# Optimization experiments

Hardware: AMD Instinct MI355X
Metric: run time of the kernel (lower is better)

## Reference

```python
import jax, jax.numpy as jnp
import numpy as np

N, VQ, VK, C, H = 4, 4096, 4096, 128, 64


def setup_inputs() -> dict:
    key = jax.random.key(0)
    kx, ky, kq, kk, kv = jax.random.split(key, 5)
    # xavier-uniform-ish scale for params
    def xavier(k, shape):
        fan_in, fan_out = shape
        lim = (6.0 / (fan_in + fan_out)) ** 0.5
        return jax.random.uniform(k, shape, jnp.float32, -lim, lim)
    return {
        "x": jax.random.normal(kx, (N, VQ, C), jnp.float32),
        "y": jax.random.normal(ky, (N, VK, C), jnp.float32),
        "Wq": xavier(kq, (C, H)),
        "Wk": xavier(kk, (C, H)),
        "Wv": xavier(kv, (C, C)),
    }


def reference(x, y, Wq, Wk, Wv):
    # x: [n, vq, c], y: [n, vk, c]
    scale = Wq.shape[1] ** (-0.5)
    q = jnp.einsum('nvc,co->nvo', x, Wq)   # [n, vq, h]
    k = jnp.einsum('nvc,co->nvo', y, Wk)   # [n, vk, h]
    v = jnp.einsum('nvc,co->nvo', y, Wv)   # [n, vk, c]
    scores = jnp.einsum('nqc,nkc->nqk', q, k) * scale  # [n, vq, vk]
    attn = jax.nn.softmax(scores, axis=-1)
    return jnp.einsum('nqk,nkc->nqc', attn, v)         # [n, vq, c]
```

## Files before the change

kernel.cpp:

```cpp
#include <hip/hip_runtime.h>

typedef __bf16 bf16x8 __attribute__((ext_vector_type(8)));
typedef __bf16 bf16x4 __attribute__((ext_vector_type(4)));
typedef __bf16 bf16x2 __attribute__((ext_vector_type(2)));
typedef float  f32x4  __attribute__((ext_vector_type(4)));
typedef float  f32x16 __attribute__((ext_vector_type(16)));
typedef int    i32x4  __attribute__((ext_vector_type(4)));

#define MFMA16 __builtin_amdgcn_mfma_f32_16x16x32_bf16
#define MFMA32 __builtin_amdgcn_mfma_f32_32x32x16_bf16

static constexpr int BATCH = 4;
static constexpr int SEQ   = 4096;
static constexpr int CDIM  = 128;
static constexpr int HDIM  = 64;
static constexpr float FIXMAX = 16.0f;

union FB2  { bf16x2 h; int i; };
union I4B8 { i32x4 i; bf16x8 b; };

__device__ inline bf16x8 load8f_cvt(const float* __restrict__ p) {
    f32x4 a = *reinterpret_cast<const f32x4*>(p);
    f32x4 b = *reinterpret_cast<const f32x4*>(p + 4);
    bf16x8 r;
    r[0] = (__bf16)a[0]; r[1] = (__bf16)a[1]; r[2] = (__bf16)a[2]; r[3] = (__bf16)a[3];
    r[4] = (__bf16)b[0]; r[5] = (__bf16)b[1]; r[6] = (__bf16)b[2]; r[7] = (__bf16)b[3];
    return r;
}


__global__ __launch_bounds__(256) void proj_all_kernel(
    const float* __restrict__ x, const float* __restrict__ y,
    const float* __restrict__ Wq, const float* __restrict__ Wk,
    const float* __restrict__ Wv,
    __bf16* __restrict__ Qw, __bf16* __restrict__ Kw, __bf16* __restrict__ Vtw,
    float qscale)
{
    __shared__ __bf16 Wt[64][136];
    __shared__ __bf16 Vtile[64][72];

    const int job = blockIdx.x >> 8;
    const int bx  = blockIdx.x & 255;
    const int t    = threadIdx.x;
    const int lane = t & 63;
    const int w    = t >> 6;
    const int m    = lane & 15;
    const int quad = lane >> 4;

    if (job <= 1) {
        const float* X    = job ? y  : x;
        const float* W    = job ? Wk : Wq;
        __bf16*      outp = job ? Kw : Qw;
        const float scale = job ? 1.0f : qscale;

        #pragma unroll
        for (int pass = 0; pass < 4; ++pass) {
            int flat = pass * 2048 + t * 8;
            int cin  = flat >> 6;
            int h0   = flat & 63;
            bf16x8 v = load8f_cvt(W + flat);
            #pragma unroll
            for (int j = 0; j < 8; ++j) Wt[h0 + j][cin] = v[j];
        }
        __syncthreads();

        const int row0 = bx * 64 + w * 16;
        bf16x8 af[4];
        #pragma unroll
        for (int kc = 0; kc < 4; ++kc)
            af[kc] = load8f_cvt(X + (long)(row0 + m) * 128 + kc * 32 + quad * 8);

        #pragma unroll
        for (int tn = 0; tn < 4; ++tn) {
            f32x4 acc = {0.f, 0.f, 0.f, 0.f};
            #pragma unroll
            for (int kc = 0; kc < 4; ++kc) {
                bf16x8 bfrag = *reinterpret_cast<const bf16x8*>(&Wt[tn * 16 + m][kc * 32 + quad * 8]);
                acc = MFMA16(af[kc], bfrag, acc, 0, 0, 0);
            }
            #pragma unroll
            for (int r = 0; r < 4; ++r) {
                int  kg   = row0 + quad * 4 + r;
                long addr = ((long)(kg >> 5) * 4 + tn) * 512
                          + ((m >> 3) * 32 + (kg & 31)) * 8 + (m & 7);
                outp[addr] = (__bf16)(acc[r] * scale);
            }
        }
    } else {
        const int cob = (job - 2) * 64;
        const int ct0 = (job - 2) * 2;

        #pragma unroll
        for (int pass = 0; pass < 4; ++pass) {
            int flat = pass * 2048 + t * 8;
            int cin  = flat >> 6;
            int co0  = flat & 63;
            bf16x8 v = load8f_cvt(Wv + cin * 128 + cob + co0);
            #pragma unroll
            for (int j = 0; j < 8; ++j) Wt[co0 + j][cin] = v[j];
        }
        __syncthreads();

        const int row0 = bx * 64 + w * 16;
        bf16x8 af[4];
        #pragma unroll
        for (int kc = 0; kc < 4; ++kc)
            af[kc] = load8f_cvt(y + (long)(row0 + m) * 128 + kc * 32 + quad * 8);

        #pragma unroll
        for (int tn = 0; tn < 4; ++tn) {
            f32x4 acc = {0.f, 0.f, 0.f, 0.f};
            #pragma unroll
            for (int kc = 0; kc < 4; ++kc) {
                bf16x8 bfrag = *reinterpret_cast<const bf16x8*>(&Wt[tn * 16 + m][kc * 32 + quad * 8]);
                acc = MFMA16(af[kc], bfrag, acc, 0, 0, 0);
            }
            bf16x4 pk;
            #pragma unroll
            for (int r = 0; r < 4; ++r) pk[r] = (__bf16)acc[r];
            *reinterpret_cast<bf16x4*>(&Vtile[tn * 16 + m][w * 16 + quad * 4]) = pk;
        }
        __syncthreads();

        #pragma unroll
        for (int pp = 0; pp < 2; ++pp) {
            int i       = pp * 256 + t;
            int c_local = i & 31;
            int hh      = (i >> 5) & 1;
            int kc2     = (i >> 6) & 1;
            int ct_l    = (i >> 7) & 1;
            int kt_l    = i >> 8;
            bf16x8 v = *reinterpret_cast<const bf16x8*>(
                &Vtile[ct_l * 32 + c_local][kt_l * 32 + kc2 * 16 + hh * 8]);
            long dst = ((long)(bx * 2 + kt_l) * 8 + (ct0 + ct_l) * 2 + kc2) * 512
                     + (hh * 32 + c_local) * 8;
            *reinterpret_cast<bf16x8*>(Vtw + dst) = v;
        }
    }
}

__global__ __launch_bounds__(512, 2) void attn_kernel(
    const __bf16* __restrict__ Qs, const __bf16* __restrict__ Ks,
    const __bf16* __restrict__ Vs, float* __restrict__ out)
{
    __shared__ __align__(16) char smem[98304];

    const int t    = threadIdx.x;
    const int lane = t & 63;
    const int w    = t >> 6;
    const int qh   = w & 1;
    const int g    = w >> 1;
    const int qc   = lane & 31;
    const int h    = lane >> 5;

    const int bx = blockIdx.x;
    const int n  = (bx >> 1) & 3;
    const int qt = (bx >> 3) * 2 + (bx & 1);
    const int q0 = qt * 64 + qh * 32;

    const long QT = (long)n * 128 + (q0 >> 5);
    bf16x8 qf[4];
    #pragma unroll
    for (int kc = 0; kc < 4; ++kc)
        qf[kc] = *reinterpret_cast<const bf16x8*>(Qs + (QT * 4 + kc) * 512 + lane * 8);

    const long KTg = (long)n * 128 + g * 32;
    const __bf16* sbase[6];
    int soff[6], sstep[6];
    if (qh == 0) {
        #pragma unroll
        for (int k = 0; k < 4; ++k) {
            sbase[k] = Ks + KTg * 2048 + k * 512 + lane * 8;
            soff[k]  = g * 4096 + k * 1024 + lane * 16;
            sstep[k] = 2048;
        }
        #pragma unroll
        for (int v2 = 0; v2 < 2; ++v2) {
            sbase[4 + v2] = Vs + KTg * 4096 + v2 * 512 + lane * 8;
            soff[4 + v2]  = 16384 + g * 8192 + v2 * 1024 + lane * 16;
            sstep[4 + v2] = 4096;
        }
    } else {
        #pragma unroll
        for (int v2 = 0; v2 < 6; ++v2) {
            sbase[v2] = Vs + KTg * 4096 + (v2 + 2) * 512 + lane * 8;
            soff[v2]  = 16384 + g * 8192 + (v2 + 2) * 1024 + lane * 16;
            sstep[v2] = 4096;
        }
    }

    f32x16 o_acc[4];
    #pragma unroll
    for (int ct = 0; ct < 4; ++ct)
        #pragma unroll
        for (int i = 0; i < 16; ++i) o_acc[ct][i] = 0.f;
    float l_a = 0.f, l_b = 0.f;

    bf16x8 stg[6];
    #pragma unroll
    for (int c = 0; c < 6; ++c) stg[c] = *reinterpret_cast<const bf16x8*>(sbase[c]);
    #pragma unroll
    for (int c = 0; c < 6; ++c) *reinterpret_cast<bf16x8*>(smem + soff[c]) = stg[c];
    #pragma unroll
    for (int c = 0; c < 6; ++c)
        stg[c] = *reinterpret_cast<const bf16x8*>(sbase[c] + sstep[c]);
    __syncthreads();

    for (int kt = 0; kt < 32; ++kt) {
        const int p = kt & 1;
        const char* bufp = smem + p * 49152;
        char*       bufn = smem + (p ^ 1) * 49152;

        if (kt < 31) {
            #pragma unroll
            for (int c = 0; c < 6; ++c)
                *reinterpret_cast<bf16x8*>(bufn + soff[c]) = stg[c];
        }
        if (kt < 30) {
            #pragma unroll
            for (int c = 0; c < 6; ++c)
                stg[c] = *reinterpret_cast<const bf16x8*>(sbase[c] + (kt + 2) * sstep[c]);
        }

        bf16x8 kf[4];
        #pragma unroll
        for (int kc = 0; kc < 4; ++kc)
            kf[kc] = *reinterpret_cast<const bf16x8*>(bufp + g * 4096 + kc * 1024 + lane * 16);

        f32x16 s;
        #pragma unroll
        for (int i = 0; i < 16; ++i) s[i] = -FIXMAX;
        #pragma unroll
        for (int kc = 0; kc < 4; ++kc)
            s = MFMA32(kf[kc], qf[kc], s, 0, 0, 0);

        int Dw[8];
        #pragma unroll
        for (int r2 = 0; r2 < 8; ++r2) {
            float p0 = __builtin_amdgcn_exp2f(s[2 * r2]);
            float p1 = __builtin_amdgcn_exp2f(s[2 * r2 + 1]);
            l_a += p0; l_b += p1;
            FB2 u; u.h[0] = (__bf16)p0; u.h[1] = (__bf16)p1;
            Dw[r2] = u.i;
        }

        #pragma unroll
        for (int kc2 = 0; kc2 < 2; ++kc2) {
            int a0 = Dw[4 * kc2 + 0], a1 = Dw[4 * kc2 + 1];
            int a2 = Dw[4 * kc2 + 2], a3 = Dw[4 * kc2 + 3];
            int r0 = __shfl_xor(a0, 32, 64);
            int r1 = __shfl_xor(a1, 32, 64);
            int r2 = __shfl_xor(a2, 32, 64);
            int r3 = __shfl_xor(a3, 32, 64);
            I4B8 pb;
            pb.i[0] = h ? r2 : a0;
            pb.i[1] = h ? r3 : a1;
            pb.i[2] = h ? a2 : r0;
            pb.i[3] = h ? a3 : r1;
            #pragma unroll
            for (int ct = 0; ct < 4; ++ct) {
                bf16x8 vf = *reinterpret_cast<const bf16x8*>(
                    bufp + 16384 + g * 8192 + (ct * 2 + kc2) * 1024 + lane * 16);
                o_acc[ct] = MFMA32(vf, pb.b, o_acc[ct], 0, 0, 0);
            }
        }
        __syncthreads();
    }

    float l_run = l_a + l_b;

    float* mg = reinterpret_cast<float*>(smem);
    for (int gg = 1; gg < 4; ++gg) {
        if (g == gg) {
            float* dst = mg + (qh * 64 + lane) * 68;
            #pragma unroll
            for (int ct = 0; ct < 4; ++ct)
                #pragma unroll
                for (int i = 0; i < 16; ++i)
                    dst[ct * 16 + i] = o_acc[ct][i];
            dst[64] = l_run;
        }
        __syncthreads();
        if (g == 0) {
            const float* src = mg + (qh * 64 + lane) * 68;
            #pragma unroll
            for (int ct = 0; ct < 4; ++ct)
                #pragma unroll
                for (int i = 0; i < 16; ++i)
                    o_acc[ct][i] += src[ct * 16 + i];
            l_run += src[64];
        }
        __syncthreads();
    }

    if (g == 0) {
        l_run += __shfl_xor(l_run, 32, 64);
        const float inv = 1.0f / l_run;
        const long row = (long)n * SEQ + q0 + qc;
        #pragma unroll
        for (int ct = 0; ct < 4; ++ct)
            #pragma unroll
            for (int rg = 0; rg < 4; ++rg) {
                f32x4 o;
                #pragma unroll
                for (int i = 0; i < 4; ++i) o[i] = o_acc[ct][rg * 4 + i] * inv;
                *reinterpret_cast<f32x4*>(out + row * CDIM + ct * 32 + rg * 8 + h * 4) = o;
            }
    }
}

extern "C" void kernel_launch(void* const* d_in, const int* in_sizes, int n_in,
                              void* d_out, int out_size, void* d_ws, size_t ws_size,
                              hipStream_t stream)
{
    const float* x  = (const float*)d_in[0];
    const float* y  = (const float*)d_in[1];
    const float* Wq = (const float*)d_in[2];
    const float* Wk = (const float*)d_in[3];
    const float* Wv = (const float*)d_in[4];
    float* out = (float*)d_out;

    __bf16* Qw  = (__bf16*)d_ws;
    __bf16* Kw  = Qw + (long)BATCH * SEQ * HDIM;
    __bf16* Vtw = Kw + (long)BATCH * SEQ * HDIM;

    const float qscale = 0.125f * 1.4426950408889634f;

    proj_all_kernel<<<dim3(1024), dim3(256), 0, stream>>>(
        x, y, Wq, Wk, Wv, Qw, Kw, Vtw, qscale);

    attn_kernel<<<dim3(256), dim3(512), 0, stream>>>(Qw, Kw, Vtw, out);
}
```

Baseline: 113.8 us.

## Load K/V fragments directly from global into registers, drop LDS staging

Replaces the cooperative shared-memory double buffer for K and V tiles with per-wave direct global loads into register fragments, ping-ponged between two register sets. This removes the LDS writes and reads and the per-iteration __syncthreads, and shrinks shared memory to the merge buffer. The cost is that each pair of q-half waves now loads the same K/V data from global/L2 separately (2x traffic), and register pressure rises, which could reduce occupancy under launch_bounds(512,2).

Measured after the change: 112.6 us. No clear change (-1.0%).

```diff
diff --git a/kernel.cpp b/kernel.cpp
--- a/kernel.cpp
+++ b/kernel.cpp
@@ -139,11 +139,51 @@
     }
 }
 
+__device__ __forceinline__ void attn_step(
+    const bf16x8 (&kf)[4], const bf16x8 (&vf)[8], const bf16x8 (&qf)[4],
+    f32x16 (&o_acc)[4], float& l_a, float& l_b, int h)
+{
+    f32x16 s;
+    #pragma unroll
+    for (int i = 0; i < 16; ++i) s[i] = -FIXMAX;
+    #pragma unroll
+    for (int kc = 0; kc < 4; ++kc)
+        s = MFMA32(kf[kc], qf[kc], s, 0, 0, 0);
+
+    int Dw[8];
+    #pragma unroll
+    for (int r2 = 0; r2 < 8; ++r2) {
+        float p0 = __builtin_amdgcn_exp2f(s[2 * r2]);
+        float p1 = __builtin_amdgcn_exp2f(s[2 * r2 + 1]);
+        l_a += p0; l_b += p1;
+        FB2 u; u.h[0] = (__bf16)p0; u.h[1] = (__bf16)p1;
+        Dw[r2] = u.i;
+    }
+
+    #pragma unroll
+    for (int kc2 = 0; kc2 < 2; ++kc2) {
+        int a0 = Dw[4 * kc2 + 0], a1 = Dw[4 * kc2 + 1];
+        int a2 = Dw[4 * kc2 + 2], a3 = Dw[4 * kc2 + 3];
+        int r0 = __shfl_xor(a0, 32, 64);
+        int r1 = __shfl_xor(a1, 32, 64);
+        int r2 = __shfl_xor(a2, 32, 64);
+        int r3 = __shfl_xor(a3, 32, 64);
+        I4B8 pb;
+        pb.i[0] = h ? r2 : a0;
+        pb.i[1] = h ? r3 : a1;
+        pb.i[2] = h ? a2 : r0;
+        pb.i[3] = h ? a3 : r1;
+        #pragma unroll
+        for (int ct = 0; ct < 4; ++ct)
+            o_acc[ct] = MFMA32(vf[ct * 2 + kc2], pb.b, o_acc[ct], 0, 0, 0);
+    }
+}
+
 __global__ __launch_bounds__(512, 2) void attn_kernel(
     const __bf16* __restrict__ Qs, const __bf16* __restrict__ Ks,
     const __bf16* __restrict__ Vs, float* __restrict__ out)
 {
-    __shared__ __align__(16) char smem[98304];
+    __shared__ float mg[2][64][68];
 
     const int t    = threadIdx.x;
     const int lane = t & 63;
@@ -164,30 +204,8 @@
     for (int kc = 0; kc < 4; ++kc)
         qf[kc] = *reinterpret_cast<const bf16x8*>(Qs + (QT * 4 + kc) * 512 + lane * 8);
 
-    const long KTg = (long)n * 128 + g * 32;
-    const __bf16* sbase[6];
-    int soff[6], sstep[6];
-    if (qh == 0) {
-        #pragma unroll
-        for (int k = 0; k < 4; ++k) {
-            sbase[k] = Ks + KTg * 2048 + k * 512 + lane * 8;
-            soff[k]  = g * 4096 + k * 1024 + lane * 16;
-            sstep[k] = 2048;
-        }
-        #pragma unroll
-        for (int v2 = 0; v2 < 2; ++v2) {
-            sbase[4 + v2] = Vs + KTg * 4096 + v2 * 512 + lane * 8;
-            soff[4 + v2]  = 16384 + g * 8192 + v2 * 1024 + lane * 16;
-            sstep[4 + v2] = 4096;
-        }
-    } else {
-        #pragma unroll
-        for (int v2 = 0; v2 < 6; ++v2) {
-            sbase[v2] = Vs + KTg * 4096 + (v2 + 2) * 512 + lane * 8;
-            soff[v2]  = 16384 + g * 8192 + (v2 + 2) * 1024 + lane * 16;
-            sstep[v2] = 4096;
-        }
-    }
+    const __bf16* kb = Ks + ((long)n * 128 + g * 32) * 2048 + lane * 8;
+    const __bf16* vb = Vs + ((long)n * 128 + g * 32) * 4096 + lane * 8;
 
     f32x16 o_acc[4];
     #pragma unroll
@@ -196,83 +214,46 @@
         for (int i = 0; i < 16; ++i) o_acc[ct][i] = 0.f;
     float l_a = 0.f, l_b = 0.f;
 
-    bf16x8 stg[6];
-    #pragma unroll
-    for (int c = 0; c < 6; ++c) stg[c] = *reinterpret_cast<const bf16x8*>(sbase[c]);
-    #pragma unroll
-    for (int c = 0; c < 6; ++c) *reinterpret_cast<bf16x8*>(smem + soff[c]) = stg[c];
-    #pragma unroll
-    for (int c = 0; c < 6; ++c)
-        stg[c] = *reinterpret_cast<const bf16x8*>(sbase[c] + sstep[c]);
-    __syncthreads();
-
-    for (int kt = 0; kt < 32; ++kt) {
-        const int p = kt & 1;
-        const char* bufp = smem + p * 49152;
-        char*       bufn = smem + (p ^ 1) * 49152;
-
-        if (kt < 31) {
-            #pragma unroll
-            for (int c = 0; c < 6; ++c)
-                *reinterpret_cast<bf16x8*>(bufn + soff[c]) = stg[c];
-        }
+    bf16x8 kfA[4], vfA[8], kfB[4], vfB[8];
+
+    #pragma unroll
+    for (int kc = 0; kc < 4; ++kc)
+        kfA[kc] = *reinterpret_cast<const bf16x8*>(kb + kc * 512);
+    #pragma unroll
+    for (int c = 0; c < 8; ++c)
+        vfA[c] = *reinterpret_cast<const bf16x8*>(vb + c * 512);
+
+    for (int kt = 0; kt < 32; kt += 2) {
+        {
+            const __bf16* kp = kb + (long)(kt + 1) * 2048;
+            const __bf16* vp = vb + (long)(kt + 1) * 4096;
+            #pragma unroll
+            for (int kc = 0; kc < 4; ++kc)
+                kfB[kc] = *reinterpret_cast<const bf16x8*>(kp + kc * 512);
+            #pragma unroll
+            for (int c = 0; c < 8; ++c)
+                vfB[c] = *reinterpret_cast<const bf16x8*>(vp + c * 512);
+        }
+        attn_step(kfA, vfA, qf, o_acc, l_a, l_b, h);
+
         if (kt < 30) {
-            #pragma unroll
-            for (int c = 0; c < 6; ++c)
-                stg[c] = *reinterpret_cast<const bf16x8*>(sbase[c] + (kt + 2) * sstep[c]);
-        }
-
-        bf16x8 kf[4];
-        #pragma unroll
-        for (int kc = 0; kc < 4; ++kc)
-            kf[kc] = *reinterpret_cast<const bf16x8*>(bufp + g * 4096 + kc * 1024 + lane * 16);
-
-        f32x16 s;
-        #pragma unroll
-        for (int i = 0; i < 16; ++i) s[i] = -FIXMAX;
-        #pragma unroll
-        for (int kc = 0; kc < 4; ++kc)
-            s = MFMA32(kf[kc], qf[kc], s, 0, 0, 0);
-
-        int Dw[8];
-        #pragma unroll
-        for (int r2 = 0; r2 < 8; ++r2) {
-            float p0 = __builtin_amdgcn_exp2f(s[2 * r2]);
-            float p1 = __builtin_amdgcn_exp2f(s[2 * r2 + 1]);
-            l_a += p0; l_b += p1;
-            FB2 u; u.h[0] = (__bf16)p0; u.h[1] = (__bf16)p1;
-            Dw[r2] = u.i;
-        }
-
-        #pragma unroll
-        for (int kc2 = 0; kc2 < 2; ++kc2) {
-            int a0 = Dw[4 * kc2 + 0], a1 = Dw[4 * kc2 + 1];
-            int a2 = Dw[4 * kc2 + 2], a3 = Dw[4 * kc2 + 3];
-            int r0 = __shfl_xor(a0, 32, 64);
-            int r1 = __shfl_xor(a1, 32, 64);
-            int r2 = __shfl_xor(a2, 32, 64);
-            int r3 = __shfl_xor(a3, 32, 64);
-            I4B8 pb;
-            pb.i[0] = h ? r2 : a0;
-            pb.i[1] = h ? r3 : a1;
-            pb.i[2] = h ? a2 : r0;
-            pb.i[3] = h ? a3 : r1;
-            #pragma unroll
-            for (int ct = 0; ct < 4; ++ct) {
-                bf16x8 vf = *reinterpret_cast<const bf16x8*>(
-                    bufp + 16384 + g * 8192 + (ct * 2 + kc2) * 1024 + lane * 16);
-                o_acc[ct] = MFMA32(vf, pb.b, o_acc[ct], 0, 0, 0);
-            }
-        }
-        __syncthreads();
+            const __bf16* kp = kb + (long)(kt + 2) * 2048;
+            const __bf16* vp = vb + (long)(kt + 2) * 4096;
+            #pragma unroll
+            for (int kc = 0; kc < 4; ++kc)
+                kfA[kc] = *reinterpret_cast<const bf16x8*>(kp + kc * 512);
+            #pragma unroll
+            for (int c = 0; c < 8; ++c)
+                vfA[c] = *reinterpret_cast<const bf16x8*>(vp + c * 512);
+        }
+        attn_step(kfB, vfB, qf, o_acc, l_a, l_b, h);
     }
 
     float l_run = l_a + l_b;
 
-    float* mg = reinterpret_cast<float*>(smem);
     for (int gg = 1; gg < 4; ++gg) {
         if (g == gg) {
-            float* dst = mg + (qh * 64 + lane) * 68;
+            float* dst = &mg[qh][lane][0];
             #pragma unroll
             for (int ct = 0; ct < 4; ++ct)
                 #pragma unroll
@@ -282,7 +263,7 @@
         }
         __syncthreads();
         if (g == 0) {
-            const float* src = mg + (qh * 64 + lane) * 68;
+            const float* src = &mg[qh][lane][0];
             #pragma unroll
             for (int ct = 0; ct < 4; ++ct)
                 #pragma unroll
```
